# Kernel tuning notes

Hardware: AMD Instinct MI355X
Metric: run time of the kernel (lower is better)

The kernel has to match this reference:

```python
import jax, jax.numpy as jnp
import numpy as np

B, S, F, H, D = 32, 512, 32, 8, 300   # batch, seq, n_features, hidden_dim, n_dim_model
FH = min(D, F)                        # flattened GRN hidden = min(n_dim_model, n_features)


def _p(key, shape, scale=0.05):
    return (jax.random.normal(key, shape) * scale).astype(jnp.float32)


def setup_inputs() -> dict:
    key = jax.random.key(0)
    ks = jax.random.split(key, 16)
    return {
        "x": jax.random.normal(ks[0], (B, S, F), dtype=jnp.float32),
        "pre_w": _p(ks[1], (F, H)), "pre_b": _p(ks[2], (F, H)),
        "sg_fc1_w": _p(ks[3], (F, H, H)), "sg_fc1_b": _p(ks[4], (F, H)),
        "sg_fc2_w": _p(ks[5], (F, H, D)), "sg_fc2_b": _p(ks[6], (F, D)),
        "sg_gate_w": _p(ks[7], (F, D, 2 * D)), "sg_gate_b": _p(ks[8], (F, 2 * D)),
        "sg_ln_g": jnp.ones((F, D), jnp.float32), "sg_ln_b": jnp.zeros((F, D), jnp.float32),
        "fl_fc1_w": _p(ks[9], (F * H, FH)), "fl_fc1_b": _p(ks[10], (FH,)),
        "fl_fc2_w": _p(ks[11], (FH, F)), "fl_fc2_b": _p(ks[12], (F,)),
        "fl_gate_w": _p(ks[13], (F, 2 * F)), "fl_gate_b": _p(ks[14], (2 * F,)),
        "fl_ln_g": jnp.ones((F,), jnp.float32), "fl_ln_b": jnp.zeros((F,), jnp.float32),
    }


def _interp_last(x, out_dim):
    # torch F.interpolate(mode='linear', align_corners=True) along the last axis
    in_dim = x.shape[-1]
    pos = jnp.arange(out_dim) * ((in_dim - 1) / (out_dim - 1))
    lo = jnp.floor(pos).astype(jnp.int32)
    hi = jnp.minimum(lo + 1, in_dim - 1)
    w = (pos - lo.astype(pos.dtype)).astype(x.dtype)
    return x[..., lo] * (1 - w) + x[..., hi] * w


def _layer_norm(x, g, b, eps=1e-5):
    m = jnp.mean(x, axis=-1, keepdims=True)
    v = jnp.var(x, axis=-1, keepdims=True)
    return (x - m) * jax.lax.rsqrt(v + eps) * g + b


def _forward(x, pre_w, pre_b, sg_fc1_w, sg_fc1_b, sg_fc2_w, sg_fc2_b,
             sg_gate_w, sg_gate_b, sg_ln_g, sg_ln_b,
             fl_fc1_w, fl_fc1_b, fl_fc2_w, fl_fc2_b, fl_gate_w, fl_gate_b,
             fl_ln_g, fl_ln_b):
    # per-feature prescaler: Linear(1, H) for each of F features, batched
    pre = x[..., None] * pre_w + pre_b                                   # [B,S,F,H]

    # per-feature GRN (H -> H -> D), batched over the feature axis f
    h = jax.nn.elu(jnp.einsum('bsfh,fhk->bsfk', pre, sg_fc1_w) + sg_fc1_b)
    h = jnp.einsum('bsfk,fkd->bsfd', h, sg_fc2_w) + sg_fc2_b             # [B,S,F,D]
    g = jnp.einsum('bsfd,fdp->bsfp', h, sg_gate_w) + sg_gate_b           # [B,S,F,2D]
    glu = g[..., :D] * jax.nn.sigmoid(g[..., D:])
    residual = _interp_last(pre, D)                                      # H -> D interpolate projection
    outputs = _layer_norm(glu + residual, sg_ln_g, sg_ln_b)              # [B,S,F,D]

    # flattened GRN on concatenated prescaler outputs (F*H -> FH -> F)
    flat = pre.reshape(pre.shape[0], pre.shape[1], F * H)                # matches torch.cat order
    fh = jax.nn.elu(flat @ fl_fc1_w + fl_fc1_b)
    fh = fh @ fl_fc2_w + fl_fc2_b                                        # [B,S,F]
    fg = fh @ fl_gate_w + fl_gate_b                                      # [B,S,2F]
    fglu = fg[..., :F] * jax.nn.sigmoid(fg[..., F:])
    wlogits = _layer_norm(fglu + _interp_last(flat, F), fl_ln_g, fl_ln_b)
    w = jax.nn.softmax(wlogits, axis=-1)                                 # [B,S,F]

    out = jnp.einsum('bsfd,bsf->bsd', outputs, w)                        # softmax-weighted sum over features
    return out, w[..., None, :]                                          # weights unsqueezed at dim -2


def reference(x, pre_w, pre_b, sg_fc1_w, sg_fc1_b, sg_fc2_w, sg_fc2_b,
              sg_gate_w, sg_gate_b, sg_ln_g, sg_ln_b,
              fl_fc1_w, fl_fc1_b, fl_fc2_w, fl_fc2_b, fl_gate_w, fl_gate_b,
              fl_ln_g, fl_ln_b):
    return _forward(x, pre_w, pre_b, sg_fc1_w, sg_fc1_b, sg_fc2_w, sg_fc2_b,
                    sg_gate_w, sg_gate_b, sg_ln_g, sg_ln_b,
                    fl_fc1_w, fl_fc1_b, fl_fc2_w, fl_fc2_b, fl_gate_w, fl_gate_b,
                    fl_ln_g, fl_ln_b)
```

## Files before the change

### kernel.cpp

```cpp
#include <hip/hip_runtime.h>
#include <hip/hip_bf16.h>

#define NB 32
#define NS 512
#define NF 32
#define NH 8
#define ND 300
#define NTOK (NB*NS)
#define TPW 8
#define WPB 4
#define TPB (TPW*WPB)

using bf16 = __hip_bfloat16;
typedef float v2f __attribute__((ext_vector_type(2)));

__device__ __forceinline__ float rcpf_(float x){ return __builtin_amdgcn_rcpf(x); }
__device__ __forceinline__ float rsqf_(float x){ return __builtin_amdgcn_rsqf(x); }
__device__ __forceinline__ float sigm(float x){ return rcpf_(1.0f + __expf(-x)); }
__device__ __forceinline__ float eluf(float x){ return x > 0.0f ? x : __expf(x) - 1.0f; }

__device__ __forceinline__ v2f fma2(v2f a, v2f b, v2f c){
    return __builtin_elementwise_fma(a, b, c);
}
__device__ __forceinline__ v2f fma2s(float s, v2f b, v2f c){
    return __builtin_elementwise_fma((v2f){s, s}, b, c);
}

template<int BF16>
__device__ __forceinline__ float ldf(const void* p, size_t i){
    if (BF16) return __bfloat162float(((const bf16*)p)[i]);
    return ((const float*)p)[i];
}
template<int BF16>
__device__ __forceinline__ void stf(void* p, size_t i, float v){
    if (BF16) ((bf16*)p)[i] = __float2bfloat16(v);
    else      ((float*)p)[i] = v;
}

__device__ __forceinline__ bool is_bf16(const void* ones){
    return *(const unsigned*)ones == 0x3F803F80u;
}

__device__ __forceinline__ v2f unpk(unsigned u){
    return (v2f){ __int_as_float((int)(u << 16)),
                  __int_as_float((int)(u & 0xFFFF0000u)) };
}
__device__ __forceinline__ unsigned pack_bf(float a, float b){
    bf16 ha = __float2bfloat16(a), hb = __float2bfloat16(b);
    return (unsigned)*(unsigned short*)&ha | ((unsigned)*(unsigned short*)&hb << 16);
}

template<int CTRL>
__device__ __forceinline__ float dppadd(float v){
    return v + __int_as_float(__builtin_amdgcn_update_dpp(
        0, __float_as_int(v), CTRL, 0xF, 0xF, true));
}
template<int CTRL>
__device__ __forceinline__ float dppmax(float v){
    return fmaxf(v, __int_as_float(__builtin_amdgcn_update_dpp(
        __float_as_int(v), __float_as_int(v), CTRL, 0xF, 0xF, false)));
}
__device__ __forceinline__ float rlane(float v, int l){
    return __int_as_float(__builtin_amdgcn_readlane(__float_as_int(v), l));
}
__device__ __forceinline__ float wsum64(float v){
    v = dppadd<0x111>(v); v = dppadd<0x112>(v); v = dppadd<0x114>(v); v = dppadd<0x118>(v);
    v = dppadd<0x142>(v); v = dppadd<0x143>(v);
    return rlane(v, 63);
}
__device__ __forceinline__ float rsum32(float v){
    v = dppadd<0x111>(v); v = dppadd<0x112>(v); v = dppadd<0x114>(v); v = dppadd<0x118>(v);
    return rlane(v, 15) + rlane(v, 31);
}
__device__ __forceinline__ float rmax32(float v){
    v = dppmax<0x111>(v); v = dppmax<0x112>(v); v = dppmax<0x114>(v); v = dppmax<0x118>(v);
    return fmaxf(rlane(v, 15), rlane(v, 31));
}

template<int BF16>
__device__ void precompute_body(const void* __restrict__ W2, const void* __restrict__ b2,
                                const void* __restrict__ Wg, const void* __restrict__ bg,
                                const void* __restrict__ sg_g, const void* __restrict__ sg_b,
                                unsigned* __restrict__ Crow,
                                float (*part)[64][18], float (*w2s)[2400], float (*b2s)[300])
{
    const int tid = threadIdx.x;
    const int l = tid & 63;
    const int q = tid >> 6;
    const int fd = blockIdx.x * 64 + l;
    const int f = fd / 300;
    const int d = fd % 300;

    const int fLo = (blockIdx.x * 64) / 300;
    const int fHi = (blockIdx.x * 64 + 63) / 300;

    for (int ff = 0; ff <= fHi - fLo; ++ff) {
        for (int idx = tid; idx < 2400; idx += 256)
            w2s[ff][idx] = ldf<BF16>(W2, (size_t)(fLo + ff) * 2400 + idx);
        for (int idx = tid; idx < 300; idx += 256)
            b2s[ff][idx] = ldf<BF16>(b2, (size_t)(fLo + ff) * 300 + idx);
    }
    __syncthreads();

    const float* myW2 = w2s[f - fLo];
    const float* myB2 = b2s[f - fLo];
    const size_t WgA = (size_t)f * 180000 + d;

    float accA[8] = {0,0,0,0,0,0,0,0};
    float accB[8] = {0,0,0,0,0,0,0,0};
    float bA = 0.f, bB = 0.f;
    for (int m = q * 75; m < q * 75 + 75; ++m) {
        float wa = ldf<BF16>(Wg, WgA + (size_t)m * 600);
        float wb = ldf<BF16>(Wg, WgA + (size_t)m * 600 + 300);
        #pragma unroll
        for (int k = 0; k < 8; ++k) {
            float w2v = myW2[k * 300 + m];
            accA[k] += w2v * wa;
            accB[k] += w2v * wb;
        }
        bA += myB2[m] * wa;
        bB += myB2[m] * wb;
    }
    #pragma unroll
    for (int k = 0; k < 8; ++k) { part[q][l][k] = accA[k]; part[q][l][8 + k] = accB[k]; }
    part[q][l][16] = bA;
    part[q][l][17] = bB;
    __syncthreads();

    unsigned* row = Crow + (size_t)fd * 12;
    for (int v = q; v < 12; v += 4) {
        if (v < 8) {
            float sA = part[0][l][v] + part[1][l][v] + part[2][l][v] + part[3][l][v];
            float sB = part[0][l][8+v] + part[1][l][8+v] + part[2][l][8+v] + part[3][l][8+v];
            row[v] = pack_bf(sA, sB);
        } else if (v == 8) {
            float s = part[0][l][16] + part[1][l][16] + part[2][l][16] + part[3][l][16];
            float bc = s + ldf<BF16>(bg, (size_t)f * 600 + d);
            row[8] = __float_as_uint(bc);
        } else if (v == 9) {
            float s = part[0][l][17] + part[1][l][17] + part[2][l][17] + part[3][l][17];
            float bc = s + ldf<BF16>(bg, (size_t)f * 600 + d + 300);
            row[9] = __float_as_uint(bc);
        } else if (v == 10) {
            row[10] = __float_as_uint(ldf<BF16>(sg_g, (size_t)f * 300 + d));
        } else {
            row[11] = __float_as_uint(ldf<BF16>(sg_b, (size_t)f * 300 + d));
        }
    }
}

__global__ void precompute_kernel(const void* __restrict__ W2, const void* __restrict__ b2,
                                  const void* __restrict__ Wg, const void* __restrict__ bg,
                                  const void* __restrict__ sg_g, const void* __restrict__ sg_b,
                                  unsigned* __restrict__ Crow)
{
    __shared__ float part[4][64][18];
    __shared__ float w2s[2][2400];
    __shared__ float b2s[2][300];
    if (is_bf16(sg_g))
        precompute_body<1>(W2, b2, Wg, bg, sg_g, sg_b, Crow, part, w2s, b2s);
    else
        precompute_body<0>(W2, b2, Wg, bg, sg_g, sg_b, Crow, part, w2s, b2s);
}

template<int BF16>
__device__ void vsn_body(const void* __restrict__ x,
                         const void* __restrict__ pre_w, const void* __restrict__ pre_b,
                         const void* __restrict__ W1,    const void* __restrict__ b1,
                         const void* __restrict__ fl1w,  const void* __restrict__ fl1b,
                         const void* __restrict__ fl2w,  const void* __restrict__ fl2b,
                         const void* __restrict__ flgw,  const void* __restrict__ flgb,
                         const void* __restrict__ flng,  const void* __restrict__ flnb,
                         const unsigned* __restrict__ Crow,
                         void* __restrict__ d_out, float* preS_, float* hS_)
{
    void* outMain = d_out;
    void* outW    = (char*)d_out + (size_t)NTOK * ND * (BF16 ? 2 : 4);

    const int tid  = threadIdx.x;
    const int wave = tid >> 6;
    const int lane = tid & 63;
    const int tokBase = blockIdx.x * TPB + wave * TPW;

    float* myPre = preS_ + wave * (TPW * 256);
    float* myH   = hS_   + wave * (TPW * 256);

    {
        float pw[4], pb[4];
        #pragma unroll
        for (int q = 0; q < 4; ++q) {
            pw[q] = ldf<BF16>(pre_w, 4 * lane + q);
            pb[q] = ldf<BF16>(pre_b, 4 * lane + q);
        }
        const int fidx = lane >> 1;
        #pragma unroll
        for (int t = 0; t < TPW; ++t) {
            float xv = ldf<BF16>(x, (size_t)(tokBase + t) * NF + fidx);
            float4 v;
            v.x = xv * pw[0] + pb[0];
            v.y = xv * pw[1] + pb[1];
            v.z = xv * pw[2] + pb[2];
            v.w = xv * pw[3] + pb[3];
            *(float4*)(&myPre[t * 256 + 4 * lane]) = v;
        }
    }

    {
        const int f  = lane >> 1;
        const int kh = (lane & 1) * 4;
        float w1r[8][4], b1r[4];
        #pragma unroll
        for (int m = 0; m < 8; ++m)
            #pragma unroll
            for (int q = 0; q < 4; ++q)
                w1r[m][q] = ldf<BF16>(W1, (size_t)(f * 8 + m) * 8 + kh + q);
        #pragma unroll
        for (int q = 0; q < 4; ++q) b1r[q] = ldf<BF16>(b1, f * 8 + kh + q);

        #pragma unroll
        for (int t = 0; t < TPW; ++t) {
            float pr[8];
            float4 pA = *(const float4*)(&myPre[t * 256 + f * 8]);
            float4 pB = *(const float4*)(&myPre[t * 256 + f * 8 + 4]);
            pr[0]=pA.x; pr[1]=pA.y; pr[2]=pA.z; pr[3]=pA.w;
            pr[4]=pB.x; pr[5]=pB.y; pr[6]=pB.z; pr[7]=pB.w;
            float a[4] = {b1r[0], b1r[1], b1r[2], b1r[3]};
            #pragma unroll
            for (int m = 0; m < 8; ++m)
                #pragma unroll
                for (int q = 0; q < 4; ++q)
                    a[q] += pr[m] * w1r[m][q];
            float4 hv4;
            hv4.x = eluf(a[0]); hv4.y = eluf(a[1]); hv4.z = eluf(a[2]); hv4.w = eluf(a[3]);
            *(float4*)(&myH[t * 256 + 4 * lane]) = hv4;
        }
    }

    const int jj = lane & 31;
    const int hB = lane >> 5;
    float wreg[TPW];
    {
        float f1b = (hB == 0) ? ldf<BF16>(fl1b, jj) : 0.0f;
        v2f p1v[4];
        #pragma unroll
        for (int g = 0; g < 4; ++g) p1v[g] = (v2f){f1b, f1b};
        for (int kg = 0; kg < 32; ++kg) {
            const int kk = hB * 128 + kg * 4;
            float4 pr[TPW];
            #pragma unroll
            for (int t = 0; t < TPW; ++t)
                pr[t] = *(const float4*)(&myPre[t * 256 + kk]);
            float w0 = ldf<BF16>(fl1w, (size_t)(kk + 0) * 32 + jj);
            float w1 = ldf<BF16>(fl1w, (size_t)(kk + 1) * 32 + jj);
            float w2 = ldf<BF16>(fl1w, (size_t)(kk + 2) * 32 + jj);
            float w3 = ldf<BF16>(fl1w, (size_t)(kk + 3) * 32 + jj);
            #pragma unroll
            for (int g = 0; g < 4; ++g) {
                p1v[g] = fma2((v2f){pr[2*g].x, pr[2*g+1].x}, (v2f){w0, w0}, p1v[g]);
                p1v[g] = fma2((v2f){pr[2*g].y, pr[2*g+1].y}, (v2f){w1, w1}, p1v[g]);
                p1v[g] = fma2((v2f){pr[2*g].z, pr[2*g+1].z}, (v2f){w2, w2}, p1v[g]);
                p1v[g] = fma2((v2f){pr[2*g].w, pr[2*g+1].w}, (v2f){w3, w3}, p1v[g]);
            }
        }
        float fhv[TPW];
        #pragma unroll
        for (int t = 0; t < TPW; ++t) {
            float p1 = (t & 1) ? p1v[t >> 1].y : p1v[t >> 1].x;
            fhv[t] = eluf(p1 + __shfl_xor(p1, 32));
        }

        float p2[TPW];
        float f2b = ldf<BF16>(fl2b, jj);
        #pragma unroll
        for (int t = 0; t < TPW; ++t) p2[t] = f2b;
        #pragma unroll
        for (int k = 0; k < 32; ++k) {
            float wv = ldf<BF16>(fl2w, k * 32 + jj);
            #pragma unroll
            for (int t = 0; t < TPW; ++t) p2[t] += rlane(fhv[t], k) * wv;
        }
        float p3[TPW];
        float fgbv = ldf<BF16>(flgb, lane);
        #pragma unroll
        for (int t = 0; t < TPW; ++t) p3[t] = fgbv;
        #pragma unroll
        for (int k = 0; k < 32; ++k) {
            float wv = ldf<BF16>(flgw, k * 64 + lane);
            #pragma unroll
            for (int t = 0; t < TPW; ++t) p3[t] += rlane(p2[t], k) * wv;
        }

        float lng = ldf<BF16>(flng, jj), lnb = ldf<BF16>(flnb, jj);
        float posB = (float)jj * (255.0f / 31.0f);
        int loB = (int)floorf(posB); loB = loB < 0 ? 0 : (loB > 254 ? 254 : loB);
        float frB = posB - (float)loB;

        #pragma unroll
        for (int t = 0; t < TPW; ++t) {
            float fgA  = __shfl(p3[t], jj);
            float fgB  = __shfl(p3[t], jj + 32);
            float fglu = fgA * sigm(fgB);
            float pl = myPre[t * 256 + loB];
            float ph = myPre[t * 256 + loB + 1];
            float tv = fglu + pl + frB * (ph - pl);
            float S1 = rsum32(tv);
            float S2 = rsum32(tv * tv);
            float mean = S1 * (1.0f / 32.0f);
            float var  = fmaxf(S2 * (1.0f / 32.0f) - mean * mean, 0.0f);
            float rs   = rsqf_(var + 1e-5f);
            float wl   = (tv - mean) * rs * lng + lnb;
            float mx   = rmax32(wl);
            float e    = __expf(wl - mx);
            float ss   = rsum32(e);
            float wv   = e * rcpf_(ss);
            wreg[t] = wv;
            if (lane < 32) stf<BF16>(outW, (size_t)(tokBase + t) * NF + lane, wv);
        }
    }

    int lo_[5]; float fr_[5];
    #pragma unroll
    for (int i = 0; i < 5; ++i) {
        int d = i * 64 + lane;
        float pos = (float)d * (7.0f / 299.0f);
        int lo = (int)floorf(pos); lo = lo < 0 ? 0 : (lo > 6 ? 6 : lo);
        lo_[i] = lo; fr_[i] = pos - (float)lo;
    }

    float acc[TPW][5];
    #pragma unroll
    for (int t = 0; t < TPW; ++t)
        #pragma unroll
        for (int i = 0; i < 5; ++i) acc[t][i] = 0.0f;

    for (int f = 0; f < NF; ++f) {
        v2f  P[5][8];
        float bcA[5], bcB[5], lgv[5], lbv[5];
        #pragma unroll
        for (int i = 0; i < 5; ++i) {
            int d = i * 64 + lane;
            bool ok = (d < ND);
            const uint4* row = (const uint4*)(Crow + ((size_t)f * ND + (ok ? d : ND - 1)) * 12);
            uint4 c0 = row[0], c1 = row[1], c2 = row[2];
            P[i][0] = unpk(c0.x); P[i][1] = unpk(c0.y);
            P[i][2] = unpk(c0.z); P[i][3] = unpk(c0.w);
            P[i][4] = unpk(c1.x); P[i][5] = unpk(c1.y);
            P[i][6] = unpk(c1.z); P[i][7] = unpk(c1.w);
            bcA[i] = __uint_as_float(c2.x);
            bcB[i] = __uint_as_float(c2.y);
            lgv[i] = __uint_as_float(c2.z);
            lbv[i] = __uint_as_float(c2.w);
        }

        #pragma unroll
        for (int t = 0; t < TPW; ++t) {
            float h[8];
            float4 h0 = *(const float4*)(&myH[t * 256 + f * 8]);
            float4 h1 = *(const float4*)(&myH[t * 256 + f * 8 + 4]);
            h[0]=h0.x; h[1]=h0.y; h[2]=h0.z; h[3]=h0.w;
            h[4]=h1.x; h[5]=h1.y; h[6]=h1.z; h[7]=h1.w;

            float tt[5], a1 = 0.f, a2 = 0.f;
            #pragma unroll
            for (int i = 0; i < 5; ++i) {
                int d = i * 64 + lane;
                bool ok = (d < ND);
                v2f g = {bcA[i], bcB[i]};
                g = fma2s(h[0], P[i][0], g);
                g = fma2s(h[1], P[i][1], g);
                g = fma2s(h[2], P[i][2], g);
                g = fma2s(h[3], P[i][3], g);
                g = fma2s(h[4], P[i][4], g);
                g = fma2s(h[5], P[i][5], g);
                g = fma2s(h[6], P[i][6], g);
                g = fma2s(h[7], P[i][7], g);
                int base = f * 8 + lo_[i];
                float pl = myPre[t * 256 + base];
                float ph = myPre[t * 256 + base + 1];
                float tv = g.x * sigm(g.y) + pl + fr_[i] * (ph - pl);
                tv = ok ? tv : 0.0f;
                tt[i] = tv; a1 += tv; a2 += tv * tv;
            }

            float S1 = wsum64(a1);
            float S2 = wsum64(a2);
            float mean = S1 * (1.0f / 300.0f);
            float var  = fmaxf(S2 * (1.0f / 300.0f) - mean * mean, 0.0f);
            float rs   = rsqf_(var + 1e-5f);
            float wf   = rlane(wreg[t], f);
            float wrs  = wf * rs;
            #pragma unroll
            for (int i = 0; i < 5; ++i) {
                int d = i * 64 + lane;
                if (d < ND) {
                    float a = wrs * lgv[i];
                    acc[t][i] += a * tt[i] + (wf * lbv[i] - a * mean);
                }
            }
        }
    }

    #pragma unroll
    for (int t = 0; t < TPW; ++t) {
        const size_t tok = (size_t)tokBase + t;
        #pragma unroll
        for (int i = 0; i < 5; ++i) {
            int d = i * 64 + lane;
            if (d < ND) stf<BF16>(outMain, tok * ND + d, acc[t][i]);
        }
    }
}

__launch_bounds__(256)
__global__ void vsn_main(const void* __restrict__ x,
                         const void* __restrict__ pre_w, const void* __restrict__ pre_b,
                         const void* __restrict__ W1,    const void* __restrict__ b1,
                         const void* __restrict__ fl1w,  const void* __restrict__ fl1b,
                         const void* __restrict__ fl2w,  const void* __restrict__ fl2b,
                         const void* __restrict__ flgw,  const void* __restrict__ flgb,
                         const void* __restrict__ flng,  const void* __restrict__ flnb,
                         const unsigned* __restrict__ Crow, void* __restrict__ d_out)
{
    __shared__ float preS_[WPB * TPW * 256];
    __shared__ float hS_[WPB * TPW * 256];
    if (is_bf16(flng))
        vsn_body<1>(x, pre_w, pre_b, W1, b1, fl1w, fl1b, fl2w, fl2b,
                    flgw, flgb, flng, flnb, Crow, d_out, preS_, hS_);
    else
        vsn_body<0>(x, pre_w, pre_b, W1, b1, fl1w, fl1b, fl2w, fl2b,
                    flgw, flgb, flng, flnb, Crow, d_out, preS_, hS_);
}

extern "C" void kernel_launch(void* const* d_in, const int* in_sizes, int n_in,
                              void* d_out, int out_size, void* d_ws, size_t ws_size,
                              hipStream_t stream)
{
    const void* x     = d_in[0];
    const void* pre_w = d_in[1];
    const void* pre_b = d_in[2];
    const void* W1    = d_in[3];
    const void* b1    = d_in[4];
    const void* W2    = d_in[5];
    const void* b2    = d_in[6];
    const void* Wg    = d_in[7];
    const void* bg    = d_in[8];
    const void* sg_g  = d_in[9];
    const void* sg_b  = d_in[10];
    const void* fl1w  = d_in[11];
    const void* fl1b  = d_in[12];
    const void* fl2w  = d_in[13];
    const void* fl2b  = d_in[14];
    const void* flgw  = d_in[15];
    const void* flgb  = d_in[16];
    const void* flng  = d_in[17];
    const void* flnb  = d_in[18];

    unsigned* Crow = (unsigned*)d_ws;

    precompute_kernel<<<150, 256, 0, stream>>>(W2, b2, Wg, bg, sg_g, sg_b, Crow);

    vsn_main<<<NTOK / TPB, 256, 0, stream>>>(x, pre_w, pre_b, W1, b1,
        fl1w, fl1b, fl2w, fl2b, flgw, flgb, flng, flnb, Crow, d_out);
}
```

Baseline: 322.6 us.

## Widen precompute grid, store GRN hidden as bf16 in LDS, refactor LN accumulate

The precompute kernel now has each block handle 16 (f,d) outputs instead of 64, splitting the 300-long m reduction across 16 thread groups and launching 600 blocks instead of 150. This raises parallelism for the folded gate-weight product, which previously ran on few CUs with long serial loops. The main kernel stores the ELU hidden activations in LDS as packed bf16, which halves that scratch space and its read traffic but rounds the hidden values to bf16. The layer-norm weighted accumulation is rewritten as fused FMAs.

```diff
diff --git a/kernel.cpp b/kernel.cpp
--- a/kernel.cpp
+++ b/kernel.cpp
@@ -82,34 +82,36 @@
                                 const void* __restrict__ Wg, const void* __restrict__ bg,
                                 const void* __restrict__ sg_g, const void* __restrict__ sg_b,
                                 unsigned* __restrict__ Crow,
-                                float (*part)[64][18], float (*w2s)[2400], float (*b2s)[300])
+                                float (*part)[16][18], float* w2s, float* b2s)
 {
     const int tid = threadIdx.x;
-    const int l = tid & 63;
-    const int q = tid >> 6;
-    const int fd = blockIdx.x * 64 + l;
+    const int l = tid & 15;
+    const int q = tid >> 4;
+    const int fd = blockIdx.x * 16 + l;
     const int f = fd / 300;
     const int d = fd % 300;
 
-    const int fLo = (blockIdx.x * 64) / 300;
-    const int fHi = (blockIdx.x * 64 + 63) / 300;
+    const int fLo = (blockIdx.x * 16) / 300;
+    const int fHi = (blockIdx.x * 16 + 15) / 300;
 
     for (int ff = 0; ff <= fHi - fLo; ++ff) {
         for (int idx = tid; idx < 2400; idx += 256)
-            w2s[ff][idx] = ldf<BF16>(W2, (size_t)(fLo + ff) * 2400 + idx);
+            w2s[ff * 2400 + idx] = ldf<BF16>(W2, (size_t)(fLo + ff) * 2400 + idx);
         for (int idx = tid; idx < 300; idx += 256)
-            b2s[ff][idx] = ldf<BF16>(b2, (size_t)(fLo + ff) * 300 + idx);
+            b2s[ff * 300 + idx] = ldf<BF16>(b2, (size_t)(fLo + ff) * 300 + idx);
     }
     __syncthreads();
 
-    const float* myW2 = w2s[f - fLo];
-    const float* myB2 = b2s[f - fLo];
+    const float* myW2 = w2s + (f - fLo) * 2400;
+    const float* myB2 = b2s + (f - fLo) * 300;
     const size_t WgA = (size_t)f * 180000 + d;
 
+    const int m0 = q * 19;
+    const int m1 = (m0 + 19 < 300) ? m0 + 19 : 300;
     float accA[8] = {0,0,0,0,0,0,0,0};
     float accB[8] = {0,0,0,0,0,0,0,0};
     float bA = 0.f, bB = 0.f;
-    for (int m = q * 75; m < q * 75 + 75; ++m) {
+    for (int m = m0; m < m1; ++m) {
         float wa = ldf<BF16>(Wg, WgA + (size_t)m * 600);
         float wb = ldf<BF16>(Wg, WgA + (size_t)m * 600 + 300);
         #pragma unroll
@@ -127,24 +129,30 @@
     part[q][l][17] = bB;
     __syncthreads();
 
-    unsigned* row = Crow + (size_t)fd * 12;
-    for (int v = q; v < 12; v += 4) {
+    if (tid < 192) {
+        const int pl_ = tid / 12, v = tid % 12;
+        const int fd2 = blockIdx.x * 16 + pl_;
+        const int f2 = fd2 / 300, d2 = fd2 % 300;
+        unsigned* row = Crow + (size_t)fd2 * 12;
         if (v < 8) {
-            float sA = part[0][l][v] + part[1][l][v] + part[2][l][v] + part[3][l][v];
-            float sB = part[0][l][8+v] + part[1][l][8+v] + part[2][l][8+v] + part[3][l][8+v];
+            float sA = 0.f, sB = 0.f;
+            #pragma unroll
+            for (int qq = 0; qq < 16; ++qq) { sA += part[qq][pl_][v]; sB += part[qq][pl_][8 + v]; }
             row[v] = pack_bf(sA, sB);
         } else if (v == 8) {
-            float s = part[0][l][16] + part[1][l][16] + part[2][l][16] + part[3][l][16];
-            float bc = s + ldf<BF16>(bg, (size_t)f * 600 + d);
-            row[8] = __float_as_uint(bc);
+            float s = 0.f;
+            #pragma unroll
+            for (int qq = 0; qq < 16; ++qq) s += part[qq][pl_][16];
+            row[8] = __float_as_uint(s + ldf<BF16>(bg, (size_t)f2 * 600 + d2));
         } else if (v == 9) {
-            float s = part[0][l][17] + part[1][l][17] + part[2][l][17] + part[3][l][17];
-            float bc = s + ldf<BF16>(bg, (size_t)f * 600 + d + 300);
-            row[9] = __float_as_uint(bc);
+            float s = 0.f;
+            #pragma unroll
+            for (int qq = 0; qq < 16; ++qq) s += part[qq][pl_][17];
+            row[9] = __float_as_uint(s + ldf<BF16>(bg, (size_t)f2 * 600 + d2 + 300));
         } else if (v == 10) {
-            row[10] = __float_as_uint(ldf<BF16>(sg_g, (size_t)f * 300 + d));
+            row[10] = __float_as_uint(ldf<BF16>(sg_g, (size_t)f2 * 300 + d2));
         } else {
-            row[11] = __float_as_uint(ldf<BF16>(sg_b, (size_t)f * 300 + d));
+            row[11] = __float_as_uint(ldf<BF16>(sg_b, (size_t)f2 * 300 + d2));
         }
     }
 }
@@ -154,9 +162,9 @@
                                   const void* __restrict__ sg_g, const void* __restrict__ sg_b,
                                   unsigned* __restrict__ Crow)
 {
-    __shared__ float part[4][64][18];
-    __shared__ float w2s[2][2400];
-    __shared__ float b2s[2][300];
+    __shared__ float part[16][16][18];
+    __shared__ float w2s[2 * 2400];
+    __shared__ float b2s[2 * 300];
     if (is_bf16(sg_g))
         precompute_body<1>(W2, b2, Wg, bg, sg_g, sg_b, Crow, part, w2s, b2s);
     else
@@ -172,7 +180,7 @@
                          const void* __restrict__ flgw,  const void* __restrict__ flgb,
                          const void* __restrict__ flng,  const void* __restrict__ flnb,
                          const unsigned* __restrict__ Crow,
-                         void* __restrict__ d_out, float* preS_, float* hS_)
+                         void* __restrict__ d_out, float* preS_, unsigned* hS_)
 {
     void* outMain = d_out;
     void* outW    = (char*)d_out + (size_t)NTOK * ND * (BF16 ? 2 : 4);
@@ -182,8 +190,8 @@
     const int lane = tid & 63;
     const int tokBase = blockIdx.x * TPB + wave * TPW;
 
-    float* myPre = preS_ + wave * (TPW * 256);
-    float* myH   = hS_   + wave * (TPW * 256);
+    float*    myPre = preS_ + wave * (TPW * 256);
+    unsigned* myH   = hS_   + wave * (TPW * 128);
 
     {
         float pw[4], pb[4];
@@ -230,9 +238,10 @@
                 #pragma unroll
                 for (int q = 0; q < 4; ++q)
                     a[q] += pr[m] * w1r[m][q];
-            float4 hv4;
-            hv4.x = eluf(a[0]); hv4.y = eluf(a[1]); hv4.z = eluf(a[2]); hv4.w = eluf(a[3]);
-            *(float4*)(&myH[t * 256 + 4 * lane]) = hv4;
+            uint2 hp;
+            hp.x = pack_bf(eluf(a[0]), eluf(a[1]));
+            hp.y = pack_bf(eluf(a[2]), eluf(a[3]));
+            *(uint2*)(&myH[t * 128 + 2 * lane]) = hp;
         }
     }
 
@@ -354,11 +363,8 @@
 
         #pragma unroll
         for (int t = 0; t < TPW; ++t) {
-            float h[8];
-            float4 h0 = *(const float4*)(&myH[t * 256 + f * 8]);
-            float4 h1 = *(const float4*)(&myH[t * 256 + f * 8 + 4]);
-            h[0]=h0.x; h[1]=h0.y; h[2]=h0.z; h[3]=h0.w;
-            h[4]=h1.x; h[5]=h1.y; h[6]=h1.z; h[7]=h1.w;
+            uint4 hp = *(const uint4*)(&myH[t * 128 + f * 4]);
+            v2f h01 = unpk(hp.x), h23 = unpk(hp.y), h45 = unpk(hp.z), h67 = unpk(hp.w);
 
             float tt[5], a1 = 0.f, a2 = 0.f;
             #pragma unroll
@@ -366,14 +372,14 @@
                 int d = i * 64 + lane;
                 bool ok = (d < ND);
                 v2f g = {bcA[i], bcB[i]};
-                g = fma2s(h[0], P[i][0], g);
-                g = fma2s(h[1], P[i][1], g);
-                g = fma2s(h[2], P[i][2], g);
-                g = fma2s(h[3], P[i][3], g);
-                g = fma2s(h[4], P[i][4], g);
-                g = fma2s(h[5], P[i][5], g);
-                g = fma2s(h[6], P[i][6], g);
-                g = fma2s(h[7], P[i][7], g);
+                g = fma2s(h01.x, P[i][0], g);
+                g = fma2s(h01.y, P[i][1], g);
+                g = fma2s(h23.x, P[i][2], g);
+                g = fma2s(h23.y, P[i][3], g);
+                g = fma2s(h45.x, P[i][4], g);
+                g = fma2s(h45.y, P[i][5], g);
+                g = fma2s(h67.x, P[i][6], g);
+                g = fma2s(h67.y, P[i][7], g);
                 int base = f * 8 + lo_[i];
                 float pl = myPre[t * 256 + base];
                 float ph = myPre[t * 256 + base + 1];
@@ -388,13 +394,14 @@
             float var  = fmaxf(S2 * (1.0f / 300.0f) - mean * mean, 0.0f);
             float rs   = rsqf_(var + 1e-5f);
             float wf   = rlane(wreg[t], f);
-            float wrs  = wf * rs;
+            float c1v  = wf * rs;
+            float c2v  = -c1v * mean;
             #pragma unroll
             for (int i = 0; i < 5; ++i) {
                 int d = i * 64 + lane;
                 if (d < ND) {
-                    float a = wrs * lgv[i];
-                    acc[t][i] += a * tt[i] + (wf * lbv[i] - a * mean);
+                    float v = fmaf(c1v, tt[i], c2v);
+                    acc[t][i] = fmaf(lgv[i], v, fmaf(wf, lbv[i], acc[t][i]));
                 }
             }
         }
@@ -421,8 +428,8 @@
                          const void* __restrict__ flng,  const void* __restrict__ flnb,
                          const unsigned* __restrict__ Crow, void* __restrict__ d_out)
 {
-    __shared__ float preS_[WPB * TPW * 256];
-    __shared__ float hS_[WPB * TPW * 256];
+    __shared__ float    preS_[WPB * TPW * 256];
+    __shared__ unsigned hS_[WPB * TPW * 128];
     if (is_bf16(flng))
         vsn_body<1>(x, pre_w, pre_b, W1, b1, fl1w, fl1b, fl2w, fl2b,
                     flgw, flgb, flng, flnb, Crow, d_out, preS_, hS_);
@@ -457,7 +464,7 @@
 
     unsigned* Crow = (unsigned*)d_ws;
 
-    precompute_kernel<<<150, 256, 0, stream>>>(W2, b2, Wg, bg, sg_g, sg_b, Crow);
+    precompute_kernel<<<600, 256, 0, stream>>>(W2, b2, Wg, bg, sg_g, sg_b, Crow);
 
     vsn_main<<<NTOK / TPB, 256, 0, stream>>>(x, pre_w, pre_b, W1, b1,
         fl1w, fl1b, fl2w, fl2b, flgw, flgb, flng, flnb, Crow, d_out);
```

Measured after the change: 317.8 us. Within noise of the previous version (-1.5%).
